# Kernel optimization log

Measured on AMD Instinct MI355X. Metric: run time of the kernel, lower is better.

## Reference

```python
import jax, jax.numpy as jnp
import numpy as np

N_HEAD = 32
N_KV_HEAD = 8
HD = 64  # head dim
N_EMBD = 2048
B, T = 2, 2048
ROPE_THETA = 10000.0


def _apply_rope(x, cos, sin):
    # x: [B, T, H, HD]; cos/sin: [T, HD//2]. Interleaved complex pairs (even, odd),
    # matching torch.view_as_complex on x.reshape(..., -1, 2).
    x0 = x[..., 0::2]
    x1 = x[..., 1::2]
    c = cos[None, :, None, :]
    s = sin[None, :, None, :]
    o0 = x0 * c - x1 * s
    o1 = x0 * s + x1 * c
    return jnp.stack([o0, o1], axis=-1).reshape(x.shape)


def setup_inputs() -> dict:
    key = jax.random.key(0)
    k1, k2, k3 = jax.random.split(key, 3)
    x = jax.random.normal(k1, (B, T, N_EMBD), dtype=jnp.float32)
    Wqkv = jax.random.normal(k2, ((N_HEAD + 2 * N_KV_HEAD) * HD, N_EMBD), dtype=jnp.float32) * 0.02
    Wproj = jax.random.normal(k3, (N_EMBD, N_EMBD), dtype=jnp.float32) * 0.02
    # precompute_freqs_cis as in llm.c (llama path)
    freqs = 1.0 / (ROPE_THETA ** (np.arange(0, HD, 2, dtype=np.float32) / HD))
    ang = np.outer(np.arange(T, dtype=np.float32), freqs)  # [T, HD//2]
    freqs_cos = jnp.asarray(np.cos(ang), dtype=jnp.float32)
    freqs_sin = jnp.asarray(np.sin(ang), dtype=jnp.float32)
    return {"x": x, "Wqkv": Wqkv, "Wproj": Wproj,
            "freqs_cos": freqs_cos, "freqs_sin": freqs_sin, "start_pos": -1}


def reference(x, Wqkv, Wproj, freqs_cos, freqs_sin, start_pos):
    Bx, Tx, C = x.shape
    n_rep = N_HEAD // N_KV_HEAD
    qkv = x @ Wqkv.T  # [B, T, (H + 2*KV)*HD]
    q = qkv[..., : N_HEAD * HD].reshape(Bx, Tx, N_HEAD, HD)
    k = qkv[..., N_HEAD * HD: (N_HEAD + N_KV_HEAD) * HD].reshape(Bx, Tx, N_KV_HEAD, HD)
    v = qkv[..., (N_HEAD + N_KV_HEAD) * HD:].reshape(Bx, Tx, N_KV_HEAD, HD)
    # RoPE on q, k
    q = _apply_rope(q, freqs_cos, freqs_sin)
    k = _apply_rope(k, freqs_cos, freqs_sin)
    # start_pos < 0: training path, no KV cache. GQA repeat of kv heads.
    k = jnp.repeat(k, n_rep, axis=2)  # [B, T, H, HD]
    v = jnp.repeat(v, n_rep, axis=2)
    q = q.transpose(0, 2, 1, 3)  # [B, H, T, HD]
    k = k.transpose(0, 2, 1, 3)
    v = v.transpose(0, 2, 1, 3)
    scale = 1.0 / np.sqrt(HD).astype(np.float32)
    scores = jnp.einsum("bhtd,bhsd->bhts", q, k) * scale  # [B, H, T, T]
    causal = jnp.tril(jnp.ones((Tx, Tx), dtype=bool))
    scores = jnp.where(causal[None, None, :, :], scores, -jnp.inf)
    att = jax.nn.softmax(scores.astype(jnp.float32), axis=-1).astype(q.dtype)
    y = jnp.einsum("bhts,bhsd->bhtd", att, v)
    y = y.transpose(0, 2, 1, 3).reshape(Bx, Tx, C)
    return y @ Wproj.T
```

## Files before the change

### kernel.cpp

```cpp
#include <hip/hip_runtime.h>
#include <hip/hip_bf16.h>
#include <cstdint>

#define NH   32
#define NKV  8
#define HD   64
#define CE   2048
#define BB   2
#define TT   2048
#define QKVD 3072
#define MM   (BB*TT)

typedef float  f32x4  __attribute__((ext_vector_type(4)));
typedef float  f32x16 __attribute__((ext_vector_type(16)));
typedef short  s16x8  __attribute__((ext_vector_type(8)));
typedef unsigned short u16;

#define AS1 __attribute__((address_space(1)))
#define AS3 __attribute__((address_space(3)))
#define GLDS16(src, dst) __builtin_amdgcn_global_load_lds( \
    (const AS1 uint32_t*)(src), (AS3 uint32_t*)(dst), 16, 0, 0)

static __device__ __forceinline__ float bf2f(u16 u) {
    union { uint32_t u; float f; } v; v.u = ((uint32_t)u) << 16; return v.f;
}
static __device__ __forceinline__ u16 f2bf(float f) {
    union { float f; uint32_t u; } v; v.f = f;
    uint32_t r = v.u + 0x7fffu + ((v.u >> 16) & 1u);
    return (u16)(r >> 16);
}
static __device__ __forceinline__ uint32_t cvtpk(float lo, float hi) {
    uint32_t r;
    asm("v_cvt_pk_bf16_f32 %0, %1, %2" : "=v"(r) : "v"(lo), "v"(hi));
    return r;
}
static __device__ __forceinline__ void plswap(uint32_t &a, uint32_t &b) {
    asm volatile("v_permlane32_swap_b32 %0, %1" : "+v"(a), "+v"(b));
}

static __device__ __forceinline__ void cvt8(const float* __restrict__ in, uint32_t* __restrict__ out) {
    const float4* p = reinterpret_cast<const float4*>(in);
    float4 a = p[0], b = p[1];
    uint4 o;
    o.x = cvtpk(a.x, a.y); o.y = cvtpk(a.z, a.w);
    o.z = cvtpk(b.x, b.y); o.w = cvtpk(b.z, b.w);
    *reinterpret_cast<uint4*>(out) = o;
}
__global__ void k_cvt_all(const float* __restrict__ x, const float* __restrict__ wqkv,
                          const float* __restrict__ wproj,
                          uint32_t* __restrict__ xo, uint32_t* __restrict__ wqo,
                          uint32_t* __restrict__ wpo,
                          const float* __restrict__ fcos, const float* __restrict__ fsin,
                          float2* __restrict__ csT) {
    const int n1 = MM * CE / 8, n2 = QKVD * CE / 8, n3 = CE * CE / 8, n4 = 32 * TT / 8;
    int i = blockIdx.x * blockDim.x + threadIdx.x;
    if (i < n1) {
        cvt8(x + (size_t)i * 8, xo + (size_t)i * 4);
    } else if (i < n1 + n2) {
        int k = i - n1;
        cvt8(wqkv + (size_t)k * 8, wqo + (size_t)k * 4);
    } else if (i < n1 + n2 + n3) {
        int k = i - n1 - n2;
        cvt8(wproj + (size_t)k * 8, wpo + (size_t)k * 4);
    } else if (i < n1 + n2 + n3 + n4) {
        int k = (i - n1 - n2 - n3) * 8;
        #pragma unroll
        for (int jj = 0; jj < 8; ++jj) {
            float2 cs; cs.x = fcos[k + jj]; cs.y = fsin[k + jj];
            csT[k + jj] = cs;
        }
    }
}

__global__ __launch_bounds__(256) void k_gemm_qkv(const u16* __restrict__ A,
                                                  const u16* __restrict__ Bm,
                                                  u16* __restrict__ Qb,
                                                  u16* __restrict__ Kb,
                                                  u16* __restrict__ Vt,
                                                  const float2* __restrict__ csT) {
    __shared__ u16 As[128 * 32];
    __shared__ u16 Bs[128 * 32];
    const int K = CE;
    const int c  = blockIdx.x + 24 * blockIdx.y;
    const int nc = (c & 7) * 96 + (c >> 3);
    const int m0 = (nc / 24) * 128;
    const int n0 = (nc % 24) * 128;

    const int tid  = threadIdx.x;
    const int w    = tid >> 6;
    const int lane = tid & 63;
    const int lr   = lane & 15, lg = lane >> 4;
    const int wm   = (w >> 1) * 64, wn = (w & 1) * 64;

    const int o0 = w * 2048 + lane * 16, o1 = o0 + 1024;
    const int ar0 = o0 >> 6, ar1 = o1 >> 6;
    const int ac0 = (o0 & 63) >> 1, ac1 = (o1 & 63) >> 1;
    const size_t aof0 = (size_t)(m0 + ar0) * K + ac0;
    const size_t aof1 = (size_t)(m0 + ar1) * K + ac1;
    const size_t bof0 = (size_t)(n0 + ar0) * K + ac0;
    const size_t bof1 = (size_t)(n0 + ar1) * K + ac1;
    u16* dA0 = &As[w * 1024];       u16* dA1 = &As[w * 1024 + 512];
    u16* dB0 = &Bs[w * 1024];       u16* dB1 = &Bs[w * 1024 + 512];

    f32x4 acc[4][4] = {};

    for (int k0 = 0; k0 < K; k0 += 32) {
        GLDS16(A  + aof0 + k0, dA0);
        GLDS16(A  + aof1 + k0, dA1);
        GLDS16(Bm + bof0 + k0, dB0);
        GLDS16(Bm + bof1 + k0, dB1);
        __syncthreads();
        s16x8 af[4], bf[4];
        #pragma unroll
        for (int i = 0; i < 4; ++i)
            af[i] = *reinterpret_cast<const s16x8*>(&As[(wm + i * 16 + lr) * 32 + lg * 8]);
        #pragma unroll
        for (int j = 0; j < 4; ++j)
            bf[j] = *reinterpret_cast<const s16x8*>(&Bs[(wn + j * 16 + lr) * 32 + lg * 8]);
        #pragma unroll
        for (int i = 0; i < 4; ++i)
            #pragma unroll
            for (int j = 0; j < 4; ++j)
                acc[i][j] = __builtin_amdgcn_mfma_f32_16x16x32_bf16(af[i], bf[j], acc[i][j], 0, 0, 0);
        __syncthreads();
    }

    const float QS = 0.18033688011112042f;
    const int bb = m0 / TT;
    const int tb = m0 - bb * TT + wm;
    #pragma unroll
    for (int i = 0; i < 4; ++i) {
        const int t0 = tb + i * 16 + lg * 4;
        #pragma unroll
        for (int j = 0; j < 4; ++j) {
            const int n = n0 + wn + j * 16 + lr;
            if (n0 < NH * HD) {
                const int hh = n >> 6, d = n & 63;
                #pragma unroll
                for (int r = 0; r < 4; ++r) {
                    const int t = t0 + r;
                    const float2 cs = csT[t * 32 + (d >> 1)];
                    float v = acc[i][j][r];
                    float p = __shfl_xor(v, 1, 64);
                    float o = ((lr & 1) ? (p * cs.y + v * cs.x) : (v * cs.x - p * cs.y)) * QS;
                    float po = __shfl_xor(o, 1, 64);
                    if (!(lr & 1))
                        *reinterpret_cast<uint32_t*>(Qb + ((size_t)((bb * NH + hh) * TT + t)) * HD + d) = cvtpk(o, po);
                }
            } else if (n0 < (NH + NKV) * HD) {
                const int fk = n - NH * HD;
                const int hh = fk >> 6, d = fk & 63;
                #pragma unroll
                for (int r = 0; r < 4; ++r) {
                    const int t = t0 + r;
                    const float2 cs = csT[t * 32 + (d >> 1)];
                    float v = acc[i][j][r];
                    float p = __shfl_xor(v, 1, 64);
                    float o = (lr & 1) ? (p * cs.y + v * cs.x) : (v * cs.x - p * cs.y);
                    float po = __shfl_xor(o, 1, 64);
                    if (!(lr & 1))
                        *reinterpret_cast<uint32_t*>(Kb + ((size_t)((bb * NKV + hh) * TT + t)) * HD + d) = cvtpk(o, po);
                }
            } else {
                const int fv = n - (NH + NKV) * HD;
                const int vh = fv >> 6, d = fv & 63;
                uint2 st;
                st.x = cvtpk(acc[i][j][0], acc[i][j][1]);
                st.y = cvtpk(acc[i][j][2], acc[i][j][3]);
                *reinterpret_cast<uint2*>(Vt + ((size_t)(bb * NKV + vh) * HD + d) * TT + t0) = st;
            }
        }
    }
}

__global__ __launch_bounds__(256) void k_gemm_bt(const u16* __restrict__ A,
                                                 const u16* __restrict__ Bm,
                                                 float* __restrict__ Cout,
                                                 int M, int N, int K) {
    __shared__ u16 As[128 * 32];
    __shared__ u16 Bs[128 * 32];
    const int c  = blockIdx.x + 16 * blockIdx.y;
    const int nc = (c & 7) * 64 + (c >> 3);
    const int m0 = (nc >> 4) * 128;
    const int n0 = (nc & 15) * 128;

    const int tid  = threadIdx.x;
    const int w    = tid >> 6;
    const int lane = tid & 63;
    const int lr   = lane & 15, lg = lane >> 4;
    const int wm   = (w >> 1) * 64, wn = (w & 1) * 64;

    const int o0 = w * 2048 + lane * 16, o1 = o0 + 1024;
    const int ar0 = o0 >> 6, ar1 = o1 >> 6;
    const int ac0 = (o0 & 63) >> 1, ac1 = (o1 & 63) >> 1;
    const size_t aof0 = (size_t)(m0 + ar0) * K + ac0;
    const size_t aof1 = (size_t)(m0 + ar1) * K + ac1;
    const size_t bof0 = (size_t)(n0 + ar0) * K + ac0;
    const size_t bof1 = (size_t)(n0 + ar1) * K + ac1;
    u16* dA0 = &As[w * 1024];       u16* dA1 = &As[w * 1024 + 512];
    u16* dB0 = &Bs[w * 1024];       u16* dB1 = &Bs[w * 1024 + 512];

    f32x4 acc[4][4] = {};

    for (int k0 = 0; k0 < K; k0 += 32) {
        GLDS16(A  + aof0 + k0, dA0);
        GLDS16(A  + aof1 + k0, dA1);
        GLDS16(Bm + bof0 + k0, dB0);
        GLDS16(Bm + bof1 + k0, dB1);
        __syncthreads();
        s16x8 af[4], bf[4];
        #pragma unroll
        for (int i = 0; i < 4; ++i)
            af[i] = *reinterpret_cast<const s16x8*>(&As[(wm + i * 16 + lr) * 32 + lg * 8]);
        #pragma unroll
        for (int j = 0; j < 4; ++j)
            bf[j] = *reinterpret_cast<const s16x8*>(&Bs[(wn + j * 16 + lr) * 32 + lg * 8]);
        #pragma unroll
        for (int i = 0; i < 4; ++i)
            #pragma unroll
            for (int j = 0; j < 4; ++j)
                acc[i][j] = __builtin_amdgcn_mfma_f32_16x16x32_bf16(af[i], bf[j], acc[i][j], 0, 0, 0);
        __syncthreads();
    }

    #pragma unroll
    for (int i = 0; i < 4; ++i)
        #pragma unroll
        for (int j = 0; j < 4; ++j)
            #pragma unroll
            for (int r = 0; r < 4; ++r) {
                int m = m0 + wm + i * 16 + lg * 4 + r;
                int n = n0 + wn + j * 16 + lr;
                __builtin_nontemporal_store(acc[i][j][r], &Cout[(size_t)m * N + n]);
            }
}

__global__ __launch_bounds__(512) void k_attn(const u16* __restrict__ Q,
                                              const u16* __restrict__ Kb,
                                              const u16* __restrict__ Vt,
                                              u16* __restrict__ Y) {
    __shared__ u16 Ks[2][4096];
    __shared__ u16 Vs[2][4096];

    const int tid = threadIdx.x;
    const int w = tid >> 6, lane = tid & 63;
    const int wv = w & 3, half = w >> 2;
    const int ql = lane & 31, hi = lane >> 5;
    const int hi16 = hi << 4;

    const int lid = (int)blockIdx.x + 8 * (int)blockIdx.y + 8 * NH * (int)blockIdx.z;
    const int kvh = lid & 7;
    const int q8  = lid >> 3;
    const int b   = q8 >> 5;
    const int s   = q8 & 31;
    const int hr  = s >> 3;
    const int u   = s & 7;
    const int h   = kvh * 4 + hr;

    const int m  = b ? (7 - u) : u;
    const int j1 = 2 * m + 1, j2 = 2 * m;
    const int jq = half ? j2 : j1;
    const int q0w  = jq * 128 + wv * 32;
    const int nt   = 2 * j1 + 2;
    const int tmxw = (q0w + 31) >> 6;
    const int qabs = q0w + ql;

    const u16* qbase = Q  + ((size_t)(b * NH  + h  ) * TT) * HD;
    const u16* kbase = Kb + ((size_t)(b * NKV + kvh) * TT) * HD;
    const u16* vbase = Vt + ((size_t)(b * NKV + kvh) * HD) * TT;

    const int o0 = w * 1024 + lane * 16;
    const int r0 = o0 >> 7;
    const int c0 = (o0 & 127) ^ ((r0 & 7) << 4);
    const size_t kof0 = (size_t)r0 * HD + (c0 >> 1);
    const size_t vof0 = (size_t)r0 * TT + (c0 >> 1);

    const char* KsB = (const char*)&Ks[0][0];
    const char* VsB = (const char*)&Vs[0][0];
    const int krb0 = (0 * 32 + ql) * 128, ksz0 = ((0 * 32 + ql) & 7) << 4;
    const int krb1 = (1 * 32 + ql) * 128, ksz1 = ((1 * 32 + ql) & 7) << 4;

    s16x8 qf[4];
    #pragma unroll
    for (int ds = 0; ds < 4; ++ds)
        qf[ds] = *reinterpret_cast<const s16x8*>(qbase + (size_t)qabs * HD + ds * 16 + 8 * hi);
    asm volatile("s_waitcnt vmcnt(0)" ::: "memory");

    GLDS16(kbase + kof0, &Ks[0][w * 512]);
    GLDS16(vbase + vof0, &Vs[0][w * 512]);

    float mrow = -1e30f, lrowp = 0.f;
    f32x16 oT0 = {}, oT1 = {};

    for (int t = 0; t < nt; ++t) {
        const int cur = t & 1;
        const int kv0 = t * 64;
        if (t + 1 < nt) {
            GLDS16(kbase + (size_t)(kv0 + 64) * HD + kof0, &Ks[cur ^ 1][w * 512]);
            GLDS16(vbase + (kv0 + 64) + vof0, &Vs[cur ^ 1][w * 512]);
            asm volatile("s_waitcnt vmcnt(2)" ::: "memory");
        } else {
            asm volatile("s_waitcnt vmcnt(0)" ::: "memory");
        }
        __builtin_amdgcn_s_barrier();
        __builtin_amdgcn_sched_barrier(0);

        if (t <= tmxw) {
            const int bufo = cur * 8192;

            f32x16 sc0 = {}, sc1 = {};
            __builtin_amdgcn_s_setprio(1);
            #pragma unroll
            for (int ds = 0; ds < 4; ++ds) {
                s16x8 k0 = *reinterpret_cast<const s16x8*>(KsB + bufo + krb0 + (((ds << 5) | hi16) ^ ksz0));
                s16x8 k1 = *reinterpret_cast<const s16x8*>(KsB + bufo + krb1 + (((ds << 5) | hi16) ^ ksz1));
                sc0 = __builtin_amdgcn_mfma_f32_32x32x16_bf16(k0, qf[ds], sc0, 0, 0, 0);
                sc1 = __builtin_amdgcn_mfma_f32_32x32x16_bf16(k1, qf[ds], sc1, 0, 0, 0);
            }
            __builtin_amdgcn_s_setprio(0);

            float p0[16], p1[16];
            #pragma unroll
            for (int r = 0; r < 16; ++r) { p0[r] = sc0[r]; p1[r] = sc1[r]; }

            if (t == tmxw) {
                const int dq = qabs - kv0 - 4 * hi;
                #pragma unroll
                for (int r = 0; r < 16; ++r) {
                    const int kr = (r & 3) + 8 * (r >> 2);
                    p0[r] = (kr      <= dq) ? p0[r] : -1e30f;
                    p1[r] = (kr + 32 <= dq) ? p1[r] : -1e30f;
                }
            }

            float tmax = fmaxf(p0[0], p1[0]);
            #pragma unroll
            for (int r = 1; r < 16; ++r) tmax = fmaxf(fmaxf(tmax, p0[r]), p1[r]);
            if (__any(tmax > mrow + 8.f)) {
                float tf = fmaxf(tmax, __shfl_xor(tmax, 32, 64));
                float mn = fmaxf(mrow, tf);
                float alpha = __builtin_amdgcn_exp2f(mrow - mn);
                mrow = mn;
                lrowp *= alpha;
                #pragma unroll
                for (int r = 0; r < 16; ++r) { oT0[r] *= alpha; oT1[r] *= alpha; }
            }

            float sum = 0.f;
            #pragma unroll
            for (int r = 0; r < 16; ++r) {
                p0[r] = __builtin_amdgcn_exp2f(p0[r] - mrow);
                p1[r] = __builtin_amdgcn_exp2f(p1[r] - mrow);
                sum += p0[r] + p1[r];
            }
            lrowp += sum;

            __builtin_amdgcn_s_setprio(1);
            #pragma unroll
            for (int ks = 0; ks < 2; ++ks) {
                uint32_t a0 = cvtpk(p0[ks * 8 + 0], p0[ks * 8 + 1]);
                uint32_t b0 = cvtpk(p0[ks * 8 + 4], p0[ks * 8 + 5]);
                plswap(a0, b0);
                uint32_t a1 = cvtpk(p0[ks * 8 + 2], p0[ks * 8 + 3]);
                uint32_t b1 = cvtpk(p0[ks * 8 + 6], p0[ks * 8 + 7]);
                plswap(a1, b1);
                union { uint32_t d[4]; s16x8 v; } pb;
                pb.d[0] = a0; pb.d[1] = a1; pb.d[2] = b0; pb.d[3] = b1;
                const int colb = (0 << 6) | (ks << 5) | hi16;
                s16x8 v0 = *reinterpret_cast<const s16x8*>(VsB + bufo + krb0 + (colb ^ ksz0));
                s16x8 v1 = *reinterpret_cast<const s16x8*>(VsB + bufo + krb1 + (colb ^ ksz1));
                oT0 = __builtin_amdgcn_mfma_f32_32x32x16_bf16(v0, pb.v, oT0, 0, 0, 0);
                oT1 = __builtin_amdgcn_mfma_f32_32x32x16_bf16(v1, pb.v, oT1, 0, 0, 0);
            }
            #pragma unroll
            for (int ks = 0; ks < 2; ++ks) {
                uint32_t a0 = cvtpk(p1[ks * 8 + 0], p1[ks * 8 + 1]);
                uint32_t b0 = cvtpk(p1[ks * 8 + 4], p1[ks * 8 + 5]);
                plswap(a0, b0);
                uint32_t a1 = cvtpk(p1[ks * 8 + 2], p1[ks * 8 + 3]);
                uint32_t b1 = cvtpk(p1[ks * 8 + 6], p1[ks * 8 + 7]);
                plswap(a1, b1);
                union { uint32_t d[4]; s16x8 v; } pb;
                pb.d[0] = a0; pb.d[1] = a1; pb.d[2] = b0; pb.d[3] = b1;
                const int colb = (1 << 6) | (ks << 5) | hi16;
                s16x8 v0 = *reinterpret_cast<const s16x8*>(VsB + bufo + krb0 + (colb ^ ksz0));
                s16x8 v1 = *reinterpret_cast<const s16x8*>(VsB + bufo + krb1 + (colb ^ ksz1));
                oT0 = __builtin_amdgcn_mfma_f32_32x32x16_bf16(v0, pb.v, oT0, 0, 0, 0);
                oT1 = __builtin_amdgcn_mfma_f32_32x32x16_bf16(v1, pb.v, oT1, 0, 0, 0);
            }
            __builtin_amdgcn_s_setprio(0);
        }

        __builtin_amdgcn_sched_barrier(0);
        __builtin_amdgcn_s_barrier();
    }

    lrowp += __shfl_xor(lrowp, 32, 64);
    const float rinv = 1.f / lrowp;
    const size_t yrow = ((size_t)(b * TT + qabs) * NH + h) * HD;
    #pragma unroll
    for (int rp = 0; rp < 8; ++rp) {
        const int d = ((2 * rp) & 3) + 8 * (rp >> 1) + 4 * hi;
        *reinterpret_cast<uint32_t*>(Y + yrow + d) =
            cvtpk(oT0[2 * rp] * rinv, oT0[2 * rp + 1] * rinv);
        *reinterpret_cast<uint32_t*>(Y + yrow + 32 + d) =
            cvtpk(oT1[2 * rp] * rinv, oT1[2 * rp + 1] * rinv);
    }
}

extern "C" void kernel_launch(void* const* d_in, const int* in_sizes, int n_in,
                              void* d_out, int out_size, void* d_ws, size_t ws_size,
                              hipStream_t stream) {
    (void)in_sizes; (void)n_in; (void)out_size; (void)ws_size;
    const float* x     = (const float*)d_in[0];
    const float* wqkv  = (const float*)d_in[1];
    const float* wproj = (const float*)d_in[2];
    const float* fcos  = (const float*)d_in[3];
    const float* fsin  = (const float*)d_in[4];

    char* ws = (char*)d_ws;
    size_t off = 0;
    auto alloc = [&](size_t bytes) { void* p = ws + off; off += (bytes + 255) & ~(size_t)255; return p; };
    u16*    Xbf  = (u16*)alloc((size_t)MM * CE * 2);
    u16*    Wqb  = (u16*)alloc((size_t)QKVD * CE * 2);
    u16*    Wpb  = (u16*)alloc((size_t)CE * CE * 2);
    u16*    Qb   = (u16*)alloc((size_t)BB * NH * TT * HD * 2);
    u16*    Kbuf = (u16*)alloc((size_t)BB * NKV * TT * HD * 2);
    u16*    Vtb  = (u16*)alloc((size_t)BB * NKV * HD * TT * 2);
    u16*    Yb   = (u16*)alloc((size_t)MM * CE * 2);
    float2* csT  = (float2*)alloc((size_t)32 * TT * sizeof(float2));

    const int ncvt = MM * CE / 8 + QKVD * CE / 8 + CE * CE / 8 + 32 * TT / 8;
    k_cvt_all<<<(ncvt + 255) / 256, 256, 0, stream>>>(x, wqkv, wproj,
                                                      (uint32_t*)Xbf, (uint32_t*)Wqb, (uint32_t*)Wpb,
                                                      fcos, fsin, csT);

    dim3 g1(QKVD / 128, MM / 128);
    k_gemm_qkv<<<g1, 256, 0, stream>>>(Xbf, Wqb, Qb, Kbuf, Vtb, csT);

    dim3 ga(8, NH, BB);
    k_attn<<<ga, 512, 0, stream>>>(Qb, Kbuf, Vtb, Yb);

    dim3 g2(CE / 128, MM / 128);
    k_gemm_bt<<<g2, 256, 0, stream>>>(Yb, Wpb, (float*)d_out, MM, CE, CE);
}
```

Baseline: 204.5 us.

## Double-buffer QKV GEMM with 256x256 tiles, swizzled LDS, 512 threads

```diff
diff --git a/kernel.cpp b/kernel.cpp
--- a/kernel.cpp
+++ b/kernel.cpp
@@ -72,75 +72,98 @@
     }
 }
 
-__global__ __launch_bounds__(256) void k_gemm_qkv(const u16* __restrict__ A,
+__global__ __launch_bounds__(512) void k_gemm_qkv(const u16* __restrict__ A,
                                                   const u16* __restrict__ Bm,
                                                   u16* __restrict__ Qb,
                                                   u16* __restrict__ Kb,
                                                   u16* __restrict__ Vt,
                                                   const float2* __restrict__ csT) {
-    __shared__ u16 As[128 * 32];
-    __shared__ u16 Bs[128 * 32];
+    __shared__ u16 Al[2][8192];
+    __shared__ u16 Bl[2][8192];
     const int K = CE;
-    const int c  = blockIdx.x + 24 * blockIdx.y;
-    const int nc = (c & 7) * 96 + (c >> 3);
-    const int m0 = (nc / 24) * 128;
-    const int n0 = (nc % 24) * 128;
+    const int n0 = blockIdx.x * 256;
+    const int m0 = blockIdx.y * 256;
 
     const int tid  = threadIdx.x;
-    const int w    = tid >> 6;
+    const int wid  = tid >> 6;
     const int lane = tid & 63;
     const int lr   = lane & 15, lg = lane >> 4;
-    const int wm   = (w >> 1) * 64, wn = (w & 1) * 64;
-
-    const int o0 = w * 2048 + lane * 16, o1 = o0 + 1024;
-    const int ar0 = o0 >> 6, ar1 = o1 >> 6;
-    const int ac0 = (o0 & 63) >> 1, ac1 = (o1 & 63) >> 1;
-    const size_t aof0 = (size_t)(m0 + ar0) * K + ac0;
-    const size_t aof1 = (size_t)(m0 + ar1) * K + ac1;
-    const size_t bof0 = (size_t)(n0 + ar0) * K + ac0;
-    const size_t bof1 = (size_t)(n0 + ar1) * K + ac1;
-    u16* dA0 = &As[w * 1024];       u16* dA1 = &As[w * 1024 + 512];
-    u16* dB0 = &Bs[w * 1024];       u16* dB1 = &Bs[w * 1024 + 512];
-
-    f32x4 acc[4][4] = {};
-
-    for (int k0 = 0; k0 < K; k0 += 32) {
-        GLDS16(A  + aof0 + k0, dA0);
-        GLDS16(A  + aof1 + k0, dA1);
-        GLDS16(Bm + bof0 + k0, dB0);
-        GLDS16(Bm + bof1 + k0, dB1);
-        __syncthreads();
-        s16x8 af[4], bf[4];
-        #pragma unroll
-        for (int i = 0; i < 4; ++i)
-            af[i] = *reinterpret_cast<const s16x8*>(&As[(wm + i * 16 + lr) * 32 + lg * 8]);
-        #pragma unroll
-        for (int j = 0; j < 4; ++j)
-            bf[j] = *reinterpret_cast<const s16x8*>(&Bs[(wn + j * 16 + lr) * 32 + lg * 8]);
-        #pragma unroll
-        for (int i = 0; i < 4; ++i)
+    const int wm2  = (wid >> 2) * 128;
+    const int wn2  = (wid & 3) * 64;
+
+    const int rloc = tid >> 2;
+    const int cb   = (tid & 3) * 16;
+    size_t aof[2], bof[2];
+    #pragma unroll
+    for (int s = 0; s < 2; ++s) {
+        const int r = s * 128 + rloc;
+        const int csw = cb ^ ((r & 3) << 4);
+        aof[s] = (size_t)(m0 + r) * K + (csw >> 1);
+        bof[s] = (size_t)(n0 + r) * K + (csw >> 1);
+    }
+
+    auto STAGE = [&](int kt, int buf) {
+        const int k0 = kt * 32;
+        char* ad = (char*)&Al[buf][0] + tid * 16;
+        char* bd = (char*)&Bl[buf][0] + tid * 16;
+        GLDS16(A  + aof[0] + k0, (u16*)ad);
+        GLDS16(A  + aof[1] + k0, (u16*)(ad + 8192));
+        GLDS16(Bm + bof[0] + k0, (u16*)bd);
+        GLDS16(Bm + bof[1] + k0, (u16*)(bd + 8192));
+    };
+
+    f32x4 acc[8][4] = {};
+    STAGE(0, 0);
+
+    const int nIter = K / 32;
+    for (int t = 0; t < nIter; ++t) {
+        if (t + 1 < nIter) {
+            STAGE(t + 1, (t + 1) & 1);
+            asm volatile("s_waitcnt vmcnt(4)" ::: "memory");
+        } else {
+            asm volatile("s_waitcnt vmcnt(0)" ::: "memory");
+        }
+        __builtin_amdgcn_s_barrier();
+        __builtin_amdgcn_sched_barrier(0);
+
+        const char* Ab = (const char*)&Al[t & 1][0];
+        const char* Bb = (const char*)&Bl[t & 1][0];
+        s16x8 bfr[4];
+        #pragma unroll
+        for (int j = 0; j < 4; ++j) {
+            const int rb = wn2 + j * 16 + lr;
+            bfr[j] = *reinterpret_cast<const s16x8*>(Bb + rb * 64 + ((lg * 16) ^ ((rb & 3) << 4)));
+        }
+        __builtin_amdgcn_s_setprio(1);
+        #pragma unroll
+        for (int i8 = 0; i8 < 8; ++i8) {
+            const int ra = wm2 + i8 * 16 + lr;
+            s16x8 af = *reinterpret_cast<const s16x8*>(Ab + ra * 64 + ((lg * 16) ^ ((ra & 3) << 4)));
             #pragma unroll
             for (int j = 0; j < 4; ++j)
-                acc[i][j] = __builtin_amdgcn_mfma_f32_16x16x32_bf16(af[i], bf[j], acc[i][j], 0, 0, 0);
-        __syncthreads();
+                acc[i8][j] = __builtin_amdgcn_mfma_f32_16x16x32_bf16(af, bfr[j], acc[i8][j], 0, 0, 0);
+        }
+        __builtin_amdgcn_s_setprio(0);
+        __builtin_amdgcn_sched_barrier(0);
+        __builtin_amdgcn_s_barrier();
     }
 
     const float QS = 0.18033688011112042f;
     const int bb = m0 / TT;
-    const int tb = m0 - bb * TT + wm;
+    const int tb = m0 - bb * TT + wm2;
     #pragma unroll
-    for (int i = 0; i < 4; ++i) {
-        const int t0 = tb + i * 16 + lg * 4;
+    for (int i8 = 0; i8 < 8; ++i8) {
+        const int t0 = tb + i8 * 16 + lg * 4;
         #pragma unroll
         for (int j = 0; j < 4; ++j) {
-            const int n = n0 + wn + j * 16 + lr;
+            const int n = n0 + wn2 + j * 16 + lr;
             if (n0 < NH * HD) {
                 const int hh = n >> 6, d = n & 63;
                 #pragma unroll
                 for (int r = 0; r < 4; ++r) {
                     const int t = t0 + r;
                     const float2 cs = csT[t * 32 + (d >> 1)];
-                    float v = acc[i][j][r];
+                    float v = acc[i8][j][r];
                     float p = __shfl_xor(v, 1, 64);
                     float o = ((lr & 1) ? (p * cs.y + v * cs.x) : (v * cs.x - p * cs.y)) * QS;
                     float po = __shfl_xor(o, 1, 64);
@@ -154,7 +177,7 @@
                 for (int r = 0; r < 4; ++r) {
                     const int t = t0 + r;
                     const float2 cs = csT[t * 32 + (d >> 1)];
-                    float v = acc[i][j][r];
+                    float v = acc[i8][j][r];
                     float p = __shfl_xor(v, 1, 64);
                     float o = (lr & 1) ? (p * cs.y + v * cs.x) : (v * cs.x - p * cs.y);
                     float po = __shfl_xor(o, 1, 64);
@@ -165,8 +188,8 @@
                 const int fv = n - (NH + NKV) * HD;
                 const int vh = fv >> 6, d = fv & 63;
                 uint2 st;
-                st.x = cvtpk(acc[i][j][0], acc[i][j][1]);
-                st.y = cvtpk(acc[i][j][2], acc[i][j][3]);
+                st.x = cvtpk(acc[i8][j][0], acc[i8][j][1]);
+                st.y = cvtpk(acc[i8][j][2], acc[i8][j][3]);
                 *reinterpret_cast<uint2*>(Vt + ((size_t)(bb * NKV + vh) * HD + d) * TT + t0) = st;
             }
         }
@@ -435,8 +458,8 @@
                                                       (uint32_t*)Xbf, (uint32_t*)Wqb, (uint32_t*)Wpb,
                                                       fcos, fsin, csT);
 
-    dim3 g1(QKVD / 128, MM / 128);
-    k_gemm_qkv<<<g1, 256, 0, stream>>>(Xbf, Wqb, Qb, Kbuf, Vtb, csT);
+    dim3 g1(QKVD / 256, MM / 256);
+    k_gemm_qkv<<<g1, 512, 0, stream>>>(Xbf, Wqb, Qb, Kbuf, Vtb, csT);
 
     dim3 ga(8, NH, BB);
     k_attn<<<ga, 512, 0, stream>>>(Qb, Kbuf, Vtb, Yb);
```

After: 247.5 us. 21.0% more time.
